# Kernel tuning notes

Hardware: AMD Instinct MI355X
Metric: run time of the kernel (lower is better)

The kernel has to match this reference:

```python
import jax, jax.numpy as jnp
import numpy as np
from jax import lax

B, L, N, D, H = 32, 128, 64, 64, 4
DH = D // H


def lstm_seq(x, Wih, Whh, b, h0, c0):
    # x: [T, B, I]; PyTorch gate order i, f, g, o; bias b = b_ih + b_hh fused.
    def step(carry, xt):
        h, c = carry
        g = xt @ Wih.T + h @ Whh.T + b  # [B, 4D]
        i, f, gg, o = jnp.split(g, 4, axis=-1)
        c = jax.nn.sigmoid(f) * c + jax.nn.sigmoid(i) * jnp.tanh(gg)
        h = jax.nn.sigmoid(o) * jnp.tanh(c)
        return (h, c), h
    _, Hs = lax.scan(step, (h0, c0), x)
    return Hs  # [T, B, D]


def encode_one(x, Wih, Whh, b, pw, pb):
    # x: [T, B, 1] single variable series; per-variable LSTM encoder + temporal attn pool
    z0 = jnp.zeros((x.shape[1], Whh.shape[1]), x.dtype)
    Hs = lstm_seq(x, Wih, Whh, b, z0, z0)        # [T, B, D]
    a = jax.nn.softmax(Hs @ pw + pb, axis=0)      # softmax over time -> [T, B]
    return jnp.einsum('tb,tbd->bd', a, Hs)        # [B, D]


def decode_one(cs, Wih, Whh, b, Wh, bh, Wc, bc, ow, ob):
    # cs: [B, D]; all-zero input sequence of length L
    h0 = jnp.tanh(cs @ Wh.T + bh)
    c0 = jnp.tanh(cs @ Wc.T + bc)
    z = jnp.zeros((L, cs.shape[0], 1), cs.dtype)
    Ys = lstm_seq(z, Wih, Whh, b, h0, c0)         # [L, B, D]
    return Ys @ ow + ob                           # [L, B]


def forward(X, enc_Wih, enc_Whh, enc_b, pool_w, pool_b,
            attn_Wqkv, attn_bqkv, attn_Wo, attn_bo,
            dec_Wih, dec_Whh, dec_b, init_h_W, init_h_b, init_c_W, init_c_b,
            out_w, out_b):
    # ---- per-variable encoders (vmapped over N distinct weight sets) ----
    Xe = jnp.transpose(X[:, :L - 1, :], (2, 1, 0))[..., None]  # [N, L-1, B, 1]
    C = jax.vmap(encode_one)(Xe, enc_Wih, enc_Whh, enc_b, pool_w, pool_b)  # [N, B, D]
    C = jnp.transpose(C, (1, 0, 2))  # [B, N, D]

    # ---- cross-variable MHSA (nn.MultiheadAttention, dropout=0) ----
    qkv = C @ attn_Wqkv.T + attn_bqkv            # [B, N, 3D]
    q, k, v = jnp.split(qkv, 3, axis=-1)
    def heads(t):
        return jnp.transpose(t.reshape(B, N, H, DH), (0, 2, 1, 3))  # [B, H, N, DH]
    q, k, v = heads(q), heads(k), heads(v)
    attn = jax.nn.softmax(jnp.einsum('bhnd,bhmd->bhnm', q, k) / np.sqrt(DH), axis=-1)
    o = jnp.einsum('bhnm,bhmd->bhnd', attn, v)
    o = jnp.transpose(o, (0, 2, 1, 3)).reshape(B, N, D)
    C_star = o @ attn_Wo.T + attn_bo             # [B, N, D]

    # ---- per-variable decoders (vmapped over N) ----
    Cs = jnp.transpose(C_star, (1, 0, 2))        # [N, B, D]
    O = jax.vmap(decode_one)(Cs, dec_Wih, dec_Whh, dec_b,
                             init_h_W, init_h_b, init_c_W, init_c_b,
                             out_w, out_b)       # [N, L, B]
    recon = jnp.transpose(O[:, :L - 1, :], (2, 1, 0))  # [B, L-1, N]
    pred = O[:, L - 1, :].T                             # [B, N]
    return recon, pred, C_star


def setup_inputs() -> dict:
    key = jax.random.key(0)
    ks = jax.random.split(key, 20)
    s = 1.0 / np.sqrt(D)
    rn = lambda k, shape: (jax.random.normal(k, shape, jnp.float32) * s)
    return {
        'X': jax.random.normal(ks[0], (B, L, N), jnp.float32),
        'enc_Wih': rn(ks[1], (N, 4 * D, 1)),
        'enc_Whh': rn(ks[2], (N, 4 * D, D)),
        'enc_b': rn(ks[3], (N, 4 * D)),
        'pool_w': rn(ks[4], (N, D)),
        'pool_b': rn(ks[5], (N,)),
        'attn_Wqkv': rn(ks[6], (3 * D, D)),
        'attn_bqkv': rn(ks[7], (3 * D,)),
        'attn_Wo': rn(ks[8], (D, D)),
        'attn_bo': rn(ks[9], (D,)),
        'dec_Wih': rn(ks[10], (N, 4 * D, 1)),
        'dec_Whh': rn(ks[11], (N, 4 * D, D)),
        'dec_b': rn(ks[12], (N, 4 * D)),
        'init_h_W': rn(ks[13], (N, D, D)),
        'init_h_b': rn(ks[14], (N, D)),
        'init_c_W': rn(ks[15], (N, D, D)),
        'init_c_b': rn(ks[16], (N, D)),
        'out_w': rn(ks[17], (N, D)),
        'out_b': rn(ks[18], (N,)),
    }


def reference(X, enc_Wih, enc_Whh, enc_b, pool_w, pool_b,
              attn_Wqkv, attn_bqkv, attn_Wo, attn_bo,
              dec_Wih, dec_Whh, dec_b, init_h_W, init_h_b, init_c_W, init_c_b,
              out_w, out_b):
    return forward(X, enc_Wih, enc_Whh, enc_b, pool_w, pool_b,
                   attn_Wqkv, attn_bqkv, attn_Wo, attn_bo,
                   dec_Wih, dec_Whh, dec_b, init_h_W, init_h_b, init_c_W, init_c_b,
                   out_w, out_b)
```

## Files before the change

kernel.cpp:

```cpp
#include <hip/hip_runtime.h>
#include <cstddef>

#define BB   32
#define LL   128
#define NN   64
#define DD   64
#define HH   4

typedef float v2f __attribute__((ext_vector_type(2)));

__device__ __forceinline__ float bcast(float v, int l) {
    return __int_as_float(__builtin_amdgcn_readlane(__float_as_int(v), l));
}
__device__ __forceinline__ float sigmoidf_(float x) {
    return 1.0f / (1.0f + __expf(-x));
}
__device__ __forceinline__ float tanhf_(float x) {
    float e = __expf(2.0f * x);
    return 1.0f - 2.0f / (e + 1.0f);
}

__device__ __forceinline__ void load_gate_rows(const float* __restrict__ W,
                                               int n, int u,
                                               v2f (&wif)[64], v2f (&wgo)[64]) {
    const float4* Ri = reinterpret_cast<const float4*>(W + ((size_t)n * 256 + u      ) * 64);
    const float4* Rf = reinterpret_cast<const float4*>(W + ((size_t)n * 256 + u +  64) * 64);
    const float4* Rg = reinterpret_cast<const float4*>(W + ((size_t)n * 256 + u + 128) * 64);
    const float4* Ro = reinterpret_cast<const float4*>(W + ((size_t)n * 256 + u + 192) * 64);
#pragma unroll
    for (int q = 0; q < 16; ++q) {
        float4 a = Ri[q], b = Rf[q];
        wif[4 * q + 0] = v2f{a.x, b.x};
        wif[4 * q + 1] = v2f{a.y, b.y};
        wif[4 * q + 2] = v2f{a.z, b.z};
        wif[4 * q + 3] = v2f{a.w, b.w};
        float4 c = Rg[q], d = Ro[q];
        wgo[4 * q + 0] = v2f{c.x, d.x};
        wgo[4 * q + 1] = v2f{c.y, d.y};
        wgo[4 * q + 2] = v2f{c.z, d.z};
        wgo[4 * q + 3] = v2f{c.w, d.w};
    }
}

__global__ __launch_bounds__(64, 1)
void enc_kernel(const float* __restrict__ X,
                const float* __restrict__ Wih,
                const float* __restrict__ Whh,
                const float* __restrict__ bias,
                const float* __restrict__ poolw,
                const float* __restrict__ poolb,
                float* __restrict__ Cws)
{
    const int n = blockIdx.x >> 5;
    const int b = blockIdx.x & 31;
    const int u = threadIdx.x;

    v2f wif[64], wgo[64];
    load_gate_rows(Whh, n, u, wif, wgo);

    const float* Bn = bias + n * 256;
    const v2f bif = {Bn[u],       Bn[u +  64]};
    const v2f bgo = {Bn[u + 128], Bn[u + 192]};
    const float* Wn = Wih + n * 256;
    const v2f xif = {Wn[u],       Wn[u +  64]};
    const v2f xgo = {Wn[u + 128], Wn[u + 192]};
    const float pwu = poolw[n * DD + u];
    const float pbn = poolb[n];

    const float x0 = X[(size_t)b * (LL * NN) + (size_t)u * NN + n];
    const float x1 = X[(size_t)b * (LL * NN) + (size_t)(u + 64) * NN + n];

    float h = 0.0f, c = 0.0f;
    float m = -1e30f, s = 0.0f, pa = 0.0f;

#pragma unroll 1
    for (int t = 0; t < LL - 1; ++t) {
        const float xt = bcast((t < 64) ? x0 : x1, t & 63);
        v2f aif = __builtin_elementwise_fma(xif, v2f{xt, xt}, bif);
        v2f ago = __builtin_elementwise_fma(xgo, v2f{xt, xt}, bgo);
#pragma unroll
        for (int k = 0; k < 64; ++k) {
            const float hk = bcast(h, k);
            const v2f hh = {hk, hk};
            aif = __builtin_elementwise_fma(wif[k], hh, aif);
            ago = __builtin_elementwise_fma(wgo[k], hh, ago);
        }
        const float gi = sigmoidf_(aif.x), gf = sigmoidf_(aif.y);
        const float gg = tanhf_(ago.x),   go = sigmoidf_(ago.y);
        c = gf * c + gi * gg;
        h = go * tanhf_(c);

        float p = h * pwu;
#pragma unroll
        for (int off = 32; off >= 1; off >>= 1) p += __shfl_xor(p, off, 64);
        const float score = p + pbn;

        const float mn   = fmaxf(m, score);
        const float corr = __expf(m - mn);
        const float wgt  = __expf(score - mn);
        s  = s * corr + wgt;
        pa = pa * corr + wgt * h;
        m  = mn;
    }

    Cws[(size_t)b * (NN * DD) + (size_t)n * DD + u] = pa / s;
}

__global__ __launch_bounds__(256)
void attn_kernel(const float* __restrict__ Cws,
                 const float* __restrict__ Wqkv,
                 const float* __restrict__ bqkv,
                 float* __restrict__ Ows)
{
    const int b = blockIdx.x >> 2;
    const int h = blockIdx.x & 3;
    const int tid = threadIdx.x;

    __shared__ float Cl[64][65];
    __shared__ float Wl[48][65];
    __shared__ float biasl[48];
    __shared__ float ql[64][17], kl[64][17], vl[64][17];
    __shared__ float sl[64][65];

    for (int i = tid; i < 64 * 64; i += 256)
        Cl[i >> 6][i & 63] = Cws[(size_t)b * (NN * DD) + i];
    for (int i = tid; i < 48 * 64; i += 256) {
        int row = i >> 6, col = i & 63;
        int grp = row >> 4, r = row & 15;
        Wl[row][col] = Wqkv[(size_t)(grp * 64 + h * 16 + r) * DD + col];
    }
    if (tid < 48) {
        int grp = tid >> 4, r = tid & 15;
        biasl[tid] = bqkv[grp * 64 + h * 16 + r];
    }
    __syncthreads();

    for (int i = tid; i < 3 * 64 * 16; i += 256) {
        int sec = i >> 10;
        int rem = i & 1023;
        int nn = rem >> 4, dh = rem & 15;
        float acc = biasl[sec * 16 + dh];
        const float* wr = &Wl[sec * 16 + dh][0];
#pragma unroll 16
        for (int k = 0; k < 64; ++k) acc = fmaf(Cl[nn][k], wr[k], acc);
        if      (sec == 0) ql[nn][dh] = acc;
        else if (sec == 1) kl[nn][dh] = acc;
        else               vl[nn][dh] = acc;
    }
    __syncthreads();

    for (int i = tid; i < 64 * 64; i += 256) {
        int nn = i >> 6, mm = i & 63;
        float acc = 0.0f;
#pragma unroll
        for (int d = 0; d < 16; ++d) acc = fmaf(ql[nn][d], kl[mm][d], acc);
        sl[nn][mm] = acc * 0.25f;
    }
    __syncthreads();

    if (tid < 64) {
        float mx = -1e30f;
        for (int mm = 0; mm < 64; ++mm) mx = fmaxf(mx, sl[tid][mm]);
        float ss = 0.0f;
        for (int mm = 0; mm < 64; ++mm) {
            float e = __expf(sl[tid][mm] - mx);
            sl[tid][mm] = e;
            ss += e;
        }
        float inv = 1.0f / ss;
        for (int mm = 0; mm < 64; ++mm) sl[tid][mm] *= inv;
    }
    __syncthreads();

    for (int i = tid; i < 64 * 16; i += 256) {
        int nn = i >> 4, dh = i & 15;
        float acc = 0.0f;
#pragma unroll 16
        for (int mm = 0; mm < 64; ++mm) acc = fmaf(sl[nn][mm], vl[mm][dh], acc);
        Ows[(size_t)b * (NN * DD) + (size_t)nn * DD + h * 16 + dh] = acc;
    }
}

__global__ __launch_bounds__(256)
void proj_kernel(const float* __restrict__ Ows,
                 const float* __restrict__ Wo,
                 const float* __restrict__ bo,
                 float* __restrict__ Cstar)
{
    const int b = blockIdx.x;
    const int tid = threadIdx.x;
    __shared__ float Ol[64][65];
    __shared__ float Wl[64][65];

    for (int i = tid; i < 64 * 64; i += 256) {
        Ol[i >> 6][i & 63] = Ows[(size_t)b * (NN * DD) + i];
        Wl[i >> 6][i & 63] = Wo[i];
    }
    __syncthreads();

    for (int i = tid; i < 64 * 64; i += 256) {
        int nn = i >> 6, d = i & 63;
        float acc = bo[d];
#pragma unroll 16
        for (int k = 0; k < 64; ++k) acc = fmaf(Ol[nn][k], Wl[d][k], acc);
        Cstar[(size_t)b * (NN * DD) + i] = acc;
    }
}

__global__ __launch_bounds__(64)
void dec_init_kernel(const float* __restrict__ Cstar,
                     const float* __restrict__ WhI,
                     const float* __restrict__ bhI,
                     const float* __restrict__ WcI,
                     const float* __restrict__ bcI,
                     float* __restrict__ H0,
                     float* __restrict__ C0)
{
    const int n = blockIdx.x >> 5;
    const int b = blockIdx.x & 31;
    const int u = threadIdx.x;

    const float cs = Cstar[(size_t)b * (NN * DD) + (size_t)n * DD + u];
    const float4* Rh = reinterpret_cast<const float4*>(WhI + ((size_t)n * DD + u) * DD);
    const float4* Rc = reinterpret_cast<const float4*>(WcI + ((size_t)n * DD + u) * DD);
    float ah = bhI[n * DD + u];
    float ac = bcI[n * DD + u];
#pragma unroll
    for (int q = 0; q < 16; ++q) {
        const float4 wh = Rh[q], wc = Rc[q];
        float k0 = bcast(cs, 4 * q + 0);
        float k1 = bcast(cs, 4 * q + 1);
        float k2 = bcast(cs, 4 * q + 2);
        float k3 = bcast(cs, 4 * q + 3);
        ah = fmaf(wh.x, k0, ah); ah = fmaf(wh.y, k1, ah);
        ah = fmaf(wh.z, k2, ah); ah = fmaf(wh.w, k3, ah);
        ac = fmaf(wc.x, k0, ac); ac = fmaf(wc.y, k1, ac);
        ac = fmaf(wc.z, k2, ac); ac = fmaf(wc.w, k3, ac);
    }
    const size_t idx = ((size_t)n * BB + b) * DD + u;
    H0[idx] = tanhf_(ah);
    C0[idx] = tanhf_(ac);
}

__global__ __launch_bounds__(64, 1)
void dec_kernel(const float* __restrict__ Whh,
                const float* __restrict__ bias,
                const float* __restrict__ ow,
                const float* __restrict__ ob,
                const float* __restrict__ H0,
                const float* __restrict__ C0,
                float* __restrict__ recon,
                float* __restrict__ pred)
{
    const int n = blockIdx.x >> 5;
    const int b = blockIdx.x & 31;
    const int u = threadIdx.x;

    v2f wif[64], wgo[64];
    load_gate_rows(Whh, n, u, wif, wgo);

    const float* Bn = bias + n * 256;
    const v2f bif = {Bn[u],       Bn[u +  64]};
    const v2f bgo = {Bn[u + 128], Bn[u + 192]};
    const float owu = ow[n * DD + u];
    const float obn = ob[n];

    const size_t idx = ((size_t)n * BB + b) * DD + u;
    float h = H0[idx];
    float c = C0[idx];

#pragma unroll 1
    for (int t = 0; t < LL; ++t) {
        v2f aif = bif, ago = bgo;
#pragma unroll
        for (int k = 0; k < 64; ++k) {
            const float hk = bcast(h, k);
            const v2f hh = {hk, hk};
            aif = __builtin_elementwise_fma(wif[k], hh, aif);
            ago = __builtin_elementwise_fma(wgo[k], hh, ago);
        }
        const float gi = sigmoidf_(aif.x), gf = sigmoidf_(aif.y);
        const float gg = tanhf_(ago.x),   go = sigmoidf_(ago.y);
        c = gf * c + gi * gg;
        h = go * tanhf_(c);

        float p = h * owu;
#pragma unroll
        for (int off = 32; off >= 1; off >>= 1) p += __shfl_xor(p, off, 64);
        if (u == 0) {
            const float y = p + obn;
            if (t < LL - 1)
                recon[(size_t)b * ((LL - 1) * NN) + (size_t)t * NN + n] = y;
            else
                pred[(size_t)b * NN + n] = y;
        }
    }
}

extern "C" void kernel_launch(void* const* d_in, const int* in_sizes, int n_in,
                              void* d_out, int out_size, void* d_ws, size_t ws_size,
                              hipStream_t stream) {
    (void)in_sizes; (void)n_in; (void)out_size; (void)ws_size;

    const float* X         = (const float*)d_in[0];
    const float* enc_Wih   = (const float*)d_in[1];
    const float* enc_Whh   = (const float*)d_in[2];
    const float* enc_b     = (const float*)d_in[3];
    const float* pool_w    = (const float*)d_in[4];
    const float* pool_b    = (const float*)d_in[5];
    const float* attn_Wqkv = (const float*)d_in[6];
    const float* attn_bqkv = (const float*)d_in[7];
    const float* attn_Wo   = (const float*)d_in[8];
    const float* attn_bo   = (const float*)d_in[9];
    const float* dec_Whh   = (const float*)d_in[11];
    const float* dec_b     = (const float*)d_in[12];
    const float* init_h_W  = (const float*)d_in[13];
    const float* init_h_b  = (const float*)d_in[14];
    const float* init_c_W  = (const float*)d_in[15];
    const float* init_c_b  = (const float*)d_in[16];
    const float* out_w     = (const float*)d_in[17];
    const float* out_b     = (const float*)d_in[18];

    float* out   = (float*)d_out;
    float* recon = out;
    float* pred  = out + (size_t)BB * (LL - 1) * NN;
    float* cstar = pred + (size_t)BB * NN;

    float* Cws = (float*)d_ws;
    float* Ows = Cws + (size_t)BB * NN * DD;
    float* H0 = Cws;
    float* C0 = Ows;

    enc_kernel<<<dim3(NN * BB), dim3(64), 0, stream>>>(
        X, enc_Wih, enc_Whh, enc_b, pool_w, pool_b, Cws);

    attn_kernel<<<dim3(BB * HH), dim3(256), 0, stream>>>(
        Cws, attn_Wqkv, attn_bqkv, Ows);

    proj_kernel<<<dim3(BB), dim3(256), 0, stream>>>(
        Ows, attn_Wo, attn_bo, cstar);

    dec_init_kernel<<<dim3(NN * BB), dim3(64), 0, stream>>>(
        cstar, init_h_W, init_h_b, init_c_W, init_c_b, H0, C0);

    dec_kernel<<<dim3(NN * BB), dim3(64), 0, stream>>>(
        dec_Whh, dec_b, out_w, out_b, H0, C0, recon, pred);
}
```

Before: 578.4 us.

## Split LSTM recurrence K-dim across four waves, two batches per block

```diff
diff --git a/kernel.cpp b/kernel.cpp
--- a/kernel.cpp
+++ b/kernel.cpp
@@ -20,29 +20,30 @@
     return 1.0f - 2.0f / (e + 1.0f);
 }
 
-__device__ __forceinline__ void load_gate_rows(const float* __restrict__ W,
-                                               int n, int u,
-                                               v2f (&wif)[64], v2f (&wgo)[64]) {
-    const float4* Ri = reinterpret_cast<const float4*>(W + ((size_t)n * 256 + u      ) * 64);
-    const float4* Rf = reinterpret_cast<const float4*>(W + ((size_t)n * 256 + u +  64) * 64);
-    const float4* Rg = reinterpret_cast<const float4*>(W + ((size_t)n * 256 + u + 128) * 64);
-    const float4* Ro = reinterpret_cast<const float4*>(W + ((size_t)n * 256 + u + 192) * 64);
-#pragma unroll
-    for (int q = 0; q < 16; ++q) {
-        float4 a = Ri[q], b = Rf[q];
-        wif[4 * q + 0] = v2f{a.x, b.x};
-        wif[4 * q + 1] = v2f{a.y, b.y};
-        wif[4 * q + 2] = v2f{a.z, b.z};
-        wif[4 * q + 3] = v2f{a.w, b.w};
-        float4 c = Rg[q], d = Ro[q];
-        wgo[4 * q + 0] = v2f{c.x, d.x};
-        wgo[4 * q + 1] = v2f{c.y, d.y};
-        wgo[4 * q + 2] = v2f{c.z, d.z};
-        wgo[4 * q + 3] = v2f{c.w, d.w};
-    }
-}
-
-__global__ __launch_bounds__(64, 1)
+#define P8(X) X(0) X(1) X(2) X(3) X(4) X(5) X(6) X(7)
+#define C4(a, e) ((e) == 0 ? (a).x : (e) == 1 ? (a).y : (e) == 2 ? (a).z : (a).w)
+
+#define KSTEP(p) {                                                            \
+    const float4 hh = hp[kp0 + (p)];                                          \
+    const v2f hA = {hh.x, hh.y}, hB = {hh.z, hh.w};                           \
+    { const float a = C4(wi[(p) >> 1], ((p) & 1) * 2);                        \
+      const float b = C4(wi[(p) >> 1], ((p) & 1) * 2 + 1);                    \
+      aci = __builtin_elementwise_fma(v2f{a, a}, hA, aci);                    \
+      aci = __builtin_elementwise_fma(v2f{b, b}, hB, aci); }                  \
+    { const float a = C4(wf[(p) >> 1], ((p) & 1) * 2);                        \
+      const float b = C4(wf[(p) >> 1], ((p) & 1) * 2 + 1);                    \
+      acf = __builtin_elementwise_fma(v2f{a, a}, hA, acf);                    \
+      acf = __builtin_elementwise_fma(v2f{b, b}, hB, acf); }                  \
+    { const float a = C4(wg[(p) >> 1], ((p) & 1) * 2);                        \
+      const float b = C4(wg[(p) >> 1], ((p) & 1) * 2 + 1);                    \
+      acg = __builtin_elementwise_fma(v2f{a, a}, hA, acg);                    \
+      acg = __builtin_elementwise_fma(v2f{b, b}, hB, acg); }                  \
+    { const float a = C4(wo[(p) >> 1], ((p) & 1) * 2);                        \
+      const float b = C4(wo[(p) >> 1], ((p) & 1) * 2 + 1);                    \
+      aco = __builtin_elementwise_fma(v2f{a, a}, hA, aco);                    \
+      aco = __builtin_elementwise_fma(v2f{b, b}, hB, aco); } }
+
+__global__ __launch_bounds__(256, 4)
 void enc_kernel(const float* __restrict__ X,
                 const float* __restrict__ Wih,
                 const float* __restrict__ Whh,
@@ -51,59 +52,95 @@
                 const float* __restrict__ poolb,
                 float* __restrict__ Cws)
 {
-    const int n = blockIdx.x >> 5;
-    const int b = blockIdx.x & 31;
-    const int u = threadIdx.x;
-
-    v2f wif[64], wgo[64];
-    load_gate_rows(Whh, n, u, wif, wgo);
+    const int n   = blockIdx.x >> 4;
+    const int bg  = blockIdx.x & 15;
+    const int b0  = 2 * bg;
+    const int tid = threadIdx.x;
+    const int w   = tid >> 6;
+    const int u   = tid & 63;
+    const int kb  = w * 16;
+    const int kp0 = w * 8;
+
+    __shared__ __align__(16) float hl_sh[128];
+    __shared__ float4 part[8][64];
+    __shared__ v2f   xs[LL];
+
+    const float* Wr = Whh + ((size_t)n * 256 + u) * 64 + kb;
+    float4 wi[4], wf[4], wg[4], wo[4];
+#pragma unroll
+    for (int q = 0; q < 4; ++q) {
+        wi[q] = *(const float4*)(Wr + 4 * q);
+        wf[q] = *(const float4*)(Wr + 64 * 64 + 4 * q);
+        wg[q] = *(const float4*)(Wr + 128 * 64 + 4 * q);
+        wo[q] = *(const float4*)(Wr + 192 * 64 + 4 * q);
+    }
 
     const float* Bn = bias + n * 256;
-    const v2f bif = {Bn[u],       Bn[u +  64]};
-    const v2f bgo = {Bn[u + 128], Bn[u + 192]};
+    const float bi_ = Bn[u], bf_ = Bn[u + 64], bg_ = Bn[u + 128], bo_ = Bn[u + 192];
     const float* Wn = Wih + n * 256;
-    const v2f xif = {Wn[u],       Wn[u +  64]};
-    const v2f xgo = {Wn[u + 128], Wn[u + 192]};
+    const float wii = Wn[u], wif_ = Wn[u + 64], wig = Wn[u + 128], wio = Wn[u + 192];
     const float pwu = poolw[n * DD + u];
     const float pbn = poolb[n];
 
-    const float x0 = X[(size_t)b * (LL * NN) + (size_t)u * NN + n];
-    const float x1 = X[(size_t)b * (LL * NN) + (size_t)(u + 64) * NN + n];
-
-    float h = 0.0f, c = 0.0f;
-    float m = -1e30f, s = 0.0f, pa = 0.0f;
+    for (int i = tid; i < LL - 1; i += 256) {
+        xs[i] = v2f{X[(size_t)b0 * (LL * NN) + (size_t)i * NN + n],
+                    X[(size_t)(b0 + 1) * (LL * NN) + (size_t)i * NN + n]};
+    }
+    if (tid < 128) hl_sh[tid] = 0.0f;
+
+    float cm = 0.0f, m = -1e30f, s_ = 0.0f, pa = 0.0f;
+    __syncthreads();
+
+    const float4* hp = (const float4*)hl_sh;
 
 #pragma unroll 1
     for (int t = 0; t < LL - 1; ++t) {
-        const float xt = bcast((t < 64) ? x0 : x1, t & 63);
-        v2f aif = __builtin_elementwise_fma(xif, v2f{xt, xt}, bif);
-        v2f ago = __builtin_elementwise_fma(xgo, v2f{xt, xt}, bgo);
-#pragma unroll
-        for (int k = 0; k < 64; ++k) {
-            const float hk = bcast(h, k);
-            const v2f hh = {hk, hk};
-            aif = __builtin_elementwise_fma(wif[k], hh, aif);
-            ago = __builtin_elementwise_fma(wgo[k], hh, ago);
+        v2f aci, acf, acg, aco;
+        if (w == 0) {
+            const v2f x01 = xs[t];
+            aci = __builtin_elementwise_fma(x01, v2f{wii, wii},  v2f{bi_, bi_});
+            acf = __builtin_elementwise_fma(x01, v2f{wif_, wif_}, v2f{bf_, bf_});
+            acg = __builtin_elementwise_fma(x01, v2f{wig, wig},  v2f{bg_, bg_});
+            aco = __builtin_elementwise_fma(x01, v2f{wio, wio},  v2f{bo_, bo_});
+        } else {
+            aci = v2f{0.f, 0.f}; acf = v2f{0.f, 0.f};
+            acg = v2f{0.f, 0.f}; aco = v2f{0.f, 0.f};
         }
-        const float gi = sigmoidf_(aif.x), gf = sigmoidf_(aif.y);
-        const float gg = tanhf_(ago.x),   go = sigmoidf_(ago.y);
-        c = gf * c + gi * gg;
-        h = go * tanhf_(c);
-
-        float p = h * pwu;
-#pragma unroll
-        for (int off = 32; off >= 1; off >>= 1) p += __shfl_xor(p, off, 64);
-        const float score = p + pbn;
-
-        const float mn   = fmaxf(m, score);
-        const float corr = __expf(m - mn);
-        const float wgt  = __expf(score - mn);
-        s  = s * corr + wgt;
-        pa = pa * corr + wgt * h;
-        m  = mn;
-    }
-
-    Cws[(size_t)b * (NN * DD) + (size_t)n * DD + u] = pa / s;
+
+        P8(KSTEP)
+
+        part[2 * w + 0][u] = float4{aci.x, acf.x, acg.x, aco.x};
+        part[2 * w + 1][u] = float4{aci.y, acf.y, acg.y, aco.y};
+        __syncthreads();
+
+        if (w < 2) {
+            const float4 ga = part[w][u],     gb = part[2 + w][u];
+            const float4 gc = part[4 + w][u], gd = part[6 + w][u];
+            const float gi = sigmoidf_(ga.x + gb.x + gc.x + gd.x);
+            const float gf = sigmoidf_(ga.y + gb.y + gc.y + gd.y);
+            const float gg = tanhf_   (ga.z + gb.z + gc.z + gd.z);
+            const float go = sigmoidf_(ga.w + gb.w + gc.w + gd.w);
+            cm = gf * cm + gi * gg;
+            const float hm = go * tanhf_(cm);
+
+            float p = hm * pwu;
+#pragma unroll
+            for (int off = 32; off >= 1; off >>= 1) p += __shfl_xor(p, off, 64);
+            const float score = p + pbn;
+            const float mn   = fmaxf(m, score);
+            const float corr = __expf(m - mn);
+            const float wgt  = __expf(score - mn);
+            s_ = s_ * corr + wgt;
+            pa = pa * corr + wgt * hm;
+            m  = mn;
+
+            hl_sh[2 * u + w] = hm;
+        }
+        __syncthreads();
+    }
+
+    if (w < 2)
+        Cws[(size_t)(b0 + w) * (NN * DD) + (size_t)n * DD + u] = pa / s_;
 }
 
 __global__ __launch_bounds__(256)
@@ -242,7 +279,7 @@
     C0[idx] = tanhf_(ac);
 }
 
-__global__ __launch_bounds__(64, 1)
+__global__ __launch_bounds__(256, 4)
 void dec_kernel(const float* __restrict__ Whh,
                 const float* __restrict__ bias,
                 const float* __restrict__ ow,
@@ -252,48 +289,84 @@
                 float* __restrict__ recon,
                 float* __restrict__ pred)
 {
-    const int n = blockIdx.x >> 5;
-    const int b = blockIdx.x & 31;
-    const int u = threadIdx.x;
-
-    v2f wif[64], wgo[64];
-    load_gate_rows(Whh, n, u, wif, wgo);
+    const int n   = blockIdx.x >> 4;
+    const int bg  = blockIdx.x & 15;
+    const int b0  = 2 * bg;
+    const int tid = threadIdx.x;
+    const int w   = tid >> 6;
+    const int u   = tid & 63;
+    const int kb  = w * 16;
+    const int kp0 = w * 8;
+
+    __shared__ __align__(16) float hl_sh[128];
+    __shared__ float4 part[8][64];
+
+    const float* Wr = Whh + ((size_t)n * 256 + u) * 64 + kb;
+    float4 wi[4], wf[4], wg[4], wo[4];
+#pragma unroll
+    for (int q = 0; q < 4; ++q) {
+        wi[q] = *(const float4*)(Wr + 4 * q);
+        wf[q] = *(const float4*)(Wr + 64 * 64 + 4 * q);
+        wg[q] = *(const float4*)(Wr + 128 * 64 + 4 * q);
+        wo[q] = *(const float4*)(Wr + 192 * 64 + 4 * q);
+    }
 
     const float* Bn = bias + n * 256;
-    const v2f bif = {Bn[u],       Bn[u +  64]};
-    const v2f bgo = {Bn[u + 128], Bn[u + 192]};
+    const float bi_ = Bn[u], bf_ = Bn[u + 64], bg_ = Bn[u + 128], bo_ = Bn[u + 192];
     const float owu = ow[n * DD + u];
     const float obn = ob[n];
 
-    const size_t idx = ((size_t)n * BB + b) * DD + u;
-    float h = H0[idx];
-    float c = C0[idx];
+    float cm = 0.0f;
+    if (w < 2) {
+        const size_t idx = ((size_t)n * BB + (b0 + w)) * DD + u;
+        hl_sh[2 * u + w] = H0[idx];
+        cm = C0[idx];
+    }
+    __syncthreads();
+
+    const float4* hp = (const float4*)hl_sh;
 
 #pragma unroll 1
     for (int t = 0; t < LL; ++t) {
-        v2f aif = bif, ago = bgo;
-#pragma unroll
-        for (int k = 0; k < 64; ++k) {
-            const float hk = bcast(h, k);
-            const v2f hh = {hk, hk};
-            aif = __builtin_elementwise_fma(wif[k], hh, aif);
-            ago = __builtin_elementwise_fma(wgo[k], hh, ago);
+        v2f aci, acf, acg, aco;
+        if (w == 0) {
+            aci = v2f{bi_, bi_}; acf = v2f{bf_, bf_};
+            acg = v2f{bg_, bg_}; aco = v2f{bo_, bo_};
+        } else {
+            aci = v2f{0.f, 0.f}; acf = v2f{0.f, 0.f};
+            acg = v2f{0.f, 0.f}; aco = v2f{0.f, 0.f};
         }
-        const float gi = sigmoidf_(aif.x), gf = sigmoidf_(aif.y);
-        const float gg = tanhf_(ago.x),   go = sigmoidf_(ago.y);
-        c = gf * c + gi * gg;
-        h = go * tanhf_(c);
-
-        float p = h * owu;
-#pragma unroll
-        for (int off = 32; off >= 1; off >>= 1) p += __shfl_xor(p, off, 64);
-        if (u == 0) {
-            const float y = p + obn;
-            if (t < LL - 1)
-                recon[(size_t)b * ((LL - 1) * NN) + (size_t)t * NN + n] = y;
-            else
-                pred[(size_t)b * NN + n] = y;
+
+        P8(KSTEP)
+
+        part[2 * w + 0][u] = float4{aci.x, acf.x, acg.x, aco.x};
+        part[2 * w + 1][u] = float4{aci.y, acf.y, acg.y, aco.y};
+        __syncthreads();
+
+        if (w < 2) {
+            const float4 ga = part[w][u],     gb = part[2 + w][u];
+            const float4 gc = part[4 + w][u], gd = part[6 + w][u];
+            const float gi = sigmoidf_(ga.x + gb.x + gc.x + gd.x);
+            const float gf = sigmoidf_(ga.y + gb.y + gc.y + gd.y);
+            const float gg = tanhf_   (ga.z + gb.z + gc.z + gd.z);
+            const float go = sigmoidf_(ga.w + gb.w + gc.w + gd.w);
+            cm = gf * cm + gi * gg;
+            const float hm = go * tanhf_(cm);
+
+            float p = hm * owu;
+#pragma unroll
+            for (int off = 32; off >= 1; off >>= 1) p += __shfl_xor(p, off, 64);
+            if (u == 0) {
+                const float y = p + obn;
+                if (t < LL - 1)
+                    recon[(size_t)(b0 + w) * ((LL - 1) * NN) + (size_t)t * NN + n] = y;
+                else
+                    pred[(size_t)(b0 + w) * NN + n] = y;
+            }
+
+            hl_sh[2 * u + w] = hm;
         }
+        __syncthreads();
     }
 }
 
@@ -331,7 +404,7 @@
     float* H0 = Cws;
     float* C0 = Ows;
 
-    enc_kernel<<<dim3(NN * BB), dim3(64), 0, stream>>>(
+    enc_kernel<<<dim3(NN * 16), dim3(256), 0, stream>>>(
         X, enc_Wih, enc_Whh, enc_b, pool_w, pool_b, Cws);
 
     attn_kernel<<<dim3(BB * HH), dim3(256), 0, stream>>>(
@@ -343,6 +416,6 @@
     dec_init_kernel<<<dim3(NN * BB), dim3(64), 0, stream>>>(
         cstar, init_h_W, init_h_b, init_c_W, init_c_b, H0, C0);
 
-    dec_kernel<<<dim3(NN * BB), dim3(64), 0, stream>>>(
+    dec_kernel<<<dim3(NN * 16), dim3(256), 0, stream>>>(
         dec_Whh, dec_b, out_w, out_b, H0, C0, recon, pred);
 }
```

Measured after the change: 1.381 ms. 139% more time.
